# Kernel optimization log

Measured on AMD Instinct MI355X. Metric: run time of the kernel, lower is better.

Reference implementation:

```python
import jax, jax.numpy as jnp
import numpy as np

B, N = 4, 512
C_IN, H, W = 1024, 48, 48
IMG_H, IMG_W = 48.0, 48.0
CNN_EMB, BOX_EMB, GCN_OUT = 512, 256, 512
ROWS, COLS = 58, 30
ALPHA = 5.0
K_EDGES = 8 * N  # edges kept per image per graph

# all directed pairs (i != j) of a fully-connected graph on N nodes
_ii, _jj = np.meshgrid(np.arange(N), np.arange(N), indexing='ij')
_m = _ii != _jj
PAIRS = jnp.asarray(np.stack([_ii[_m], _jj[_m]], axis=1).astype(np.int32))  # [E,2]


def setup_inputs():
    key = jax.random.key(0)
    ks = jax.random.split(key, 12)
    x = jax.random.normal(ks[0], (B, C_IN, H, W), jnp.float32)
    # valid boxes (x1<x2, y1<y2) inside the 48x48 feature map
    p = jax.random.uniform(ks[1], (B, N, 2, 2), minval=0.0, maxval=float(W) - 2.0)
    lo = jnp.min(p, axis=2)
    hi = jnp.max(p, axis=2) + 1.0
    boxes = jnp.concatenate([lo, hi], axis=-1)  # [B,N,4] x1,y1,x2,y2

    def lin(k, fi, fo):
        return jax.random.normal(k, (fi, fo), jnp.float32) / np.sqrt(fi)

    return {
        'input': x, 'boxes': boxes,
        'im_scales': jnp.ones((B,), jnp.float32),
        'pdls': jnp.zeros((B,), jnp.float32),
        'pdts': jnp.zeros((B,), jnp.float32),
        'W_dec': jax.random.normal(ks[2], (256, C_IN, 3, 3), jnp.float32) / np.sqrt(C_IN * 9.0),
        'b_dec': jnp.zeros((256,), jnp.float32),
        'W_box': lin(ks[3], 4, BOX_EMB), 'b_box': jnp.zeros((BOX_EMB,), jnp.float32),
        'W_cnn': lin(ks[4], 256 * 4, CNN_EMB), 'b_cnn': jnp.zeros((CNN_EMB,), jnp.float32),
        'W_grow': lin(ks[5], CNN_EMB + BOX_EMB, GCN_OUT), 'b_grow': jnp.zeros((GCN_OUT,), jnp.float32),
        'W_gcol': lin(ks[6], CNN_EMB + BOX_EMB, GCN_OUT), 'b_gcol': jnp.zeros((GCN_OUT,), jnp.float32),
        'W_rcls': lin(ks[7], GCN_OUT, 2 * (ROWS - 1) * 2), 'b_rcls': jnp.zeros((2 * (ROWS - 1) * 2,), jnp.float32),
        'W_ccls': lin(ks[8], GCN_OUT, 2 * (COLS - 1) * 2), 'b_ccls': jnp.zeros((2 * (COLS - 1) * 2,), jnp.float32),
    }


def _bilinear(feat, bidx, py, px):
    # feat [B,C,H,W]; py,px [M,4] sample coords -> [M,4,C]
    Hh, Ww = feat.shape[2], feat.shape[3]
    py = jnp.clip(py, 0.0, Hh - 1.0)
    px = jnp.clip(px, 0.0, Ww - 1.0)
    y0 = jnp.floor(py).astype(jnp.int32)
    x0 = jnp.floor(px).astype(jnp.int32)
    y1 = jnp.minimum(y0 + 1, Hh - 1)
    x1 = jnp.minimum(x0 + 1, Ww - 1)
    wy = (py - y0)[..., None]
    wx = (px - x0)[..., None]
    b = bidx[:, None]
    f00 = feat[b, :, y0, x0]
    f01 = feat[b, :, y0, x1]
    f10 = feat[b, :, y1, x0]
    f11 = feat[b, :, y1, x1]
    return f00 * (1 - wy) * (1 - wx) + f01 * (1 - wy) * wx + f10 * wy * (1 - wx) + f11 * wy * wx


def _roi_align_2x2(feat, boxes, bidx):
    # roi_align output_size=2, spatial_scale=1, one sample per bin (bin center)
    x1, y1, x2, y2 = boxes[:, 0], boxes[:, 1], boxes[:, 2], boxes[:, 3]
    bw = (x2 - x1) / 2.0
    bh = (y2 - y1) / 2.0
    offs = jnp.array([0.5, 1.5], jnp.float32)
    sx = x1[:, None] + offs * bw[:, None]  # [M,2]
    sy = y1[:, None] + offs * bh[:, None]
    py = sy[:, jnp.array([0, 0, 1, 1])]  # (iy, ix) ordering
    px = sx[:, jnp.array([0, 1, 0, 1])]
    val = _bilinear(feat, bidx, py, px)  # [M,4,C]
    return jnp.transpose(val, (0, 2, 1)).reshape(val.shape[0], -1)  # [M, C*2*2]


def _edge_attrs(boxes_i, scale, pdl, pdt):
    org = (boxes_i - jnp.stack([pdl, pdt, pdl, pdt])) / scale
    cx = (org[:, 0] + org[:, 2]) * 0.5
    cy = (org[:, 1] + org[:, 3]) * 0.5
    tb_w = jnp.max(org[:, jnp.array([0, 2])])
    tb_h = jnp.max(org[:, jnp.array([1, 3])])
    s, d = PAIRS[:, 0], PAIRS[:, 1]
    row_attr = jnp.exp(-jnp.square((cy[s] - cy[d]) * ALPHA / tb_h))
    col_attr = jnp.exp(-jnp.square((cx[s] - cx[d]) * ALPHA / tb_w))
    rv, ri = jax.lax.top_k(row_attr, K_EDGES)
    cv, ci = jax.lax.top_k(col_attr, K_EDGES)
    return rv, PAIRS[ri], cv, PAIRS[ci]


def _gcn(x, Wg, bg, edges, ew, num_nodes):
    # PyG GCNConv: self-loops with weight 1, symmetric normalization
    loop = jnp.arange(num_nodes, dtype=edges.dtype)
    src = jnp.concatenate([edges[0], loop])
    dst = jnp.concatenate([edges[1], loop])
    w = jnp.concatenate([ew, jnp.ones((num_nodes,), ew.dtype)])
    deg = jax.ops.segment_sum(w, dst, num_segments=num_nodes)
    dis = jax.lax.rsqrt(deg)  # deg >= 1 thanks to self-loops
    norm = dis[src] * w * dis[dst]
    xw = x @ Wg
    agg = jax.ops.segment_sum(norm[:, None] * xw[src], dst, num_segments=num_nodes)
    return agg + bg


def _forward(input, boxes, im_scales, pdls, pdts, W_dec, b_dec, W_box, b_box,
             W_cnn, b_cnn, W_grow, b_grow, W_gcol, b_gcol, W_rcls, b_rcls, W_ccls, b_ccls):
    Bn = B * N
    flat = boxes.reshape(Bn, 4)
    # box features (relative center / size)
    cx = (flat[:, 0] + flat[:, 2]) / 2.0
    cy = (flat[:, 1] + flat[:, 3]) / 2.0
    bf = jnp.stack([cx / IMG_W, cy / IMG_H,
                    (flat[:, 2] - flat[:, 0]) / IMG_W,
                    (flat[:, 3] - flat[:, 1]) / IMG_H], axis=1)
    box_feat = jax.nn.relu(bf @ W_box + b_box)
    # decode conv + relu
    dec = jax.lax.conv_general_dilated(input, W_dec, (1, 1), 'SAME',
                                       dimension_numbers=('NCHW', 'OIHW', 'NCHW'))
    dec = jax.nn.relu(dec + b_dec[None, :, None, None])
    # roi-align 2x2 + cnn embedding
    bidx = jnp.repeat(jnp.arange(B, dtype=jnp.int32), N)
    cnn = _roi_align_2x2(dec, flat, bidx)
    cnn_feat = jax.nn.relu(cnn @ W_cnn + b_cnn)
    # per-image dense graph -> top-8N row/col edges
    rv, re, cv, ce = jax.vmap(_edge_attrs)(boxes, im_scales, pdls, pdts)
    off = (jnp.arange(B, dtype=jnp.int32) * N)[:, None, None]
    row_edge = (re + off).reshape(-1, 2).T  # [2, B*K]
    col_edge = (ce + off).reshape(-1, 2).T
    row_w = rv.reshape(-1)
    col_w = cv.reshape(-1)
    fusion = jnp.concatenate([box_feat, cnn_feat], axis=1)  # [Bn, 768]
    row_feat = jax.nn.relu(_gcn(fusion, W_grow, b_grow, row_edge, row_w, Bn))
    col_feat = jax.nn.relu(_gcn(fusion, W_gcol, b_gcol, col_edge, col_w, Bn))
    row_score = jax.nn.leaky_relu(row_feat @ W_rcls + b_rcls, 0.01).reshape(Bn, 2, ROWS - 1, 2)
    col_score = jax.nn.leaky_relu(col_feat @ W_ccls + b_ccls, 0.01).reshape(Bn, 2, COLS - 1, 2)
    return row_score, col_score


def reference(input, boxes, im_scales, pdls, pdts, W_dec, b_dec, W_box, b_box,
              W_cnn, b_cnn, W_grow, b_grow, W_gcol, b_gcol, W_rcls, b_rcls, W_ccls, b_ccls):
    return _forward(input, boxes, im_scales, pdls, pdts, W_dec, b_dec, W_box, b_box,
                    W_cnn, b_cnn, W_grow, b_grow, W_gcol, b_gcol,
                    W_rcls, b_rcls, W_ccls, b_ccls)
```

## Files before the change

kernel.cpp:

```cpp
#include <hip/hip_runtime.h>
#include <cstdint>
#include <math.h>

typedef unsigned int u32;
typedef unsigned long long u64;
typedef unsigned short ushort;

typedef __attribute__((ext_vector_type(8))) _Float16 f16x8;
typedef __attribute__((ext_vector_type(4))) _Float16 f16x4;
typedef __attribute__((ext_vector_type(4))) float f32x4;

#define NB    4
#define BnN   2048
#define NE    261632
#define NCHUNK 32
#define ECHUNK 8176
#define KEDGE 4096
#define TIECAP 2048
#define PSLICE 2359296
#define MS    64
#define TS    64

#define GLD16(gsrc, ldst)                                                    \
    __builtin_amdgcn_global_load_lds(                                        \
        (const __attribute__((address_space(1))) void*)(gsrc),               \
        (__attribute__((address_space(3))) void*)(ldst), 16, 0, 0)

__global__ __launch_bounds__(256) void prep_kernel(
    const float* __restrict__ in, _Float16* __restrict__ xf,
    const float* __restrict__ W, _Float16* __restrict__ wf,
    const float* __restrict__ Wc,  _Float16* __restrict__ WcT,
    const float* __restrict__ Wgr, _Float16* __restrict__ WgrT,
    const float* __restrict__ Wgc, _Float16* __restrict__ WgcT,
    const float* __restrict__ Wr,  _Float16* __restrict__ WrT,
    const float* __restrict__ Wcc, _Float16* __restrict__ WccT)
{
    __shared__ _Float16 sh[9216];
    const int bid = blockIdx.x;
    const int tid = threadIdx.x;
    if (bid < 3072) {
        _Float16 (*shx)[49] = (_Float16(*)[49])sh;
        int cg = bid & 15, rem = bid >> 4;
        int y = rem % 48, b = rem / 48;
        for (int i = tid; i < 64 * 48; i += 256) {
            int cl = i / 48, x = i - cl * 48;
            shx[cl][x] = (_Float16)in[(((size_t)b * 1024 + cg * 64 + cl) * 48 + y) * 48 + x];
        }
        __syncthreads();
        for (int i = tid; i < 64 * 48; i += 256) {
            int x = i / 64, cl = i - x * 64;
            xf[((size_t)(b * 48 + y) * 48 + x) * 1024 + cg * 64 + cl] = shx[cl][x];
        }
    } else if (bid < 3328) {
        int o = bid - 3072;
        for (int g = tid; g < 9216; g += 256)
            sh[g] = (_Float16)W[(size_t)o * 9216 + g];
        __syncthreads();
        for (int g = tid; g < 9216; g += 256) {
            int tap = g >> 10, ch = g & 1023;
            wf[(size_t)o * 9216 + g] = sh[ch * 9 + tap];
        }
    } else {
        _Float16 (*sht)[33] = (_Float16(*)[33])sh;
        int b2 = bid - 3328;
        const float* inm; _Float16* outm; int K, N, tx0, ty0, ntx;
        if (b2 < 512)       { inm = Wc;  outm = WcT;  K = 1024; N = 512; ntx = 16; b2 -= 0;    }
        else if (b2 < 896)  { inm = Wgr; outm = WgrT; K = 768;  N = 512; ntx = 16; b2 -= 512;  }
        else if (b2 < 1280) { inm = Wgc; outm = WgcT; K = 768;  N = 512; ntx = 16; b2 -= 896;  }
        else if (b2 < 1408) { inm = Wr;  outm = WrT;  K = 512;  N = 228; ntx = 8;  b2 -= 1280; }
        else                { inm = Wcc; outm = WccT; K = 512;  N = 116; ntx = 4;  b2 -= 1408; }
        tx0 = (b2 % ntx) * 32;
        ty0 = (b2 / ntx) * 32;
        int tx = tid & 31, ty = tid >> 5;
#pragma unroll
        for (int i = 0; i < 4; ++i) {
            int k = ty0 + ty + i * 8, n = tx0 + tx;
            sht[ty + i * 8][tx] = (k < K && n < N) ? (_Float16)inm[(size_t)k * N + n] : (_Float16)0.f;
        }
        __syncthreads();
#pragma unroll
        for (int i = 0; i < 4; ++i) {
            int n = tx0 + ty + i * 8, k = ty0 + tx;
            if (n < N && k < K) outm[(size_t)n * K + k] = sht[tx][ty + i * 8];
        }
    }
}

#define STAGE(cc)                                                            \
    {                                                                        \
        _Pragma("unroll")                                                    \
        for (int it = 0; it < 5; ++it) {                                     \
            if (it * 256 + wv * 64 < 1152)                                   \
                GLD16(wsrc[it] + (cc), &wS[(it * 256 + wv * 64) * 8]);       \
        }                                                                    \
        _Pragma("unroll")                                                    \
        for (int it = 0; it < 8; ++it)                                       \
            GLD16(xsrc[it] + (cc), &xS[(it * 256 + wv * 64) * 8]);           \
    }

#define LDB(BUF, R)                                                          \
    {                                                                        \
        _Pragma("unroll")                                                    \
        for (int u = 0; u < 9; ++u) {                                        \
            int nt_ = u / 3, dx_ = u % 3;                                    \
            BUF[u] = *(const f16x8*)&xS[(((R) * 4 + q) * 50 + nt_ * 16 + n + dx_) * 8]; \
        }                                                                    \
    }

#define DOTAP(TAP, BLO, BHI)                                                 \
    {                                                                        \
        _Pragma("unroll")                                                    \
        for (int dx_ = 0; dx_ < 3; ++dx_) {                                  \
            f16x8 a0 = *(const f16x8*)&wS[(((TAP) + dx_) * 128 + q * 32 + n) * 8];      \
            f16x8 a1 = *(const f16x8*)&wS[(((TAP) + dx_) * 128 + q * 32 + 16 + n) * 8]; \
            _Pragma("unroll")                                                \
            for (int nt_ = 0; nt_ < 3; ++nt_) {                              \
                f16x8 blo = BLO[nt_ * 3 + dx_];                              \
                f16x8 bhi = BHI[nt_ * 3 + dx_];                              \
                acc[0][0][nt_] = __builtin_amdgcn_mfma_f32_16x16x32_f16(a0, blo, acc[0][0][nt_], 0, 0, 0); \
                acc[1][0][nt_] = __builtin_amdgcn_mfma_f32_16x16x32_f16(a1, blo, acc[1][0][nt_], 0, 0, 0); \
                acc[0][1][nt_] = __builtin_amdgcn_mfma_f32_16x16x32_f16(a0, bhi, acc[0][1][nt_], 0, 0, 0); \
                acc[1][1][nt_] = __builtin_amdgcn_mfma_f32_16x16x32_f16(a1, bhi, acc[1][1][nt_], 0, 0, 0); \
            }                                                                \
        }                                                                    \
    }

__global__ __launch_bounds__(256, 3) void conv_part_kernel(
    const _Float16* __restrict__ xf, const _Float16* __restrict__ wf,
    const _Float16* __restrict__ zbuf, float* __restrict__ pbuf)
{
    __shared__ _Float16 wS[1152 * 8];
    __shared__ _Float16 xS[2048 * 8];
    const int p = blockIdx.x;
    const int L = (p & 7) * 96 + (p >> 3);
    const int og = L & 7;
    const int t  = L >> 3;
    const int xt = t % 6;
    const int bz = t / 6;
    const int y0 = xt * 8;
    const int b  = bz >> 2, ks = bz & 3;
    const int tid = threadIdx.x;
    const int wv = tid >> 6;
    const int ln = tid & 63;
    const int n  = ln & 15;
    const int q  = ln >> 4;

    f32x4 acc[2][2][3];
#pragma unroll
    for (int mt = 0; mt < 2; ++mt)
#pragma unroll
        for (int rr = 0; rr < 2; ++rr)
#pragma unroll
            for (int nt = 0; nt < 3; ++nt) acc[mt][rr][nt] = (f32x4){0.f, 0.f, 0.f, 0.f};

    const _Float16* wsrc[5];
    const _Float16* xsrc[8];
#pragma unroll
    for (int it = 0; it < 5; ++it) {
        int g = it * 256 + tid;
        int gg = (g < 1152) ? g : 0;
        int tap = gg >> 7, r = gg & 127, qq = r >> 5, oc = r & 31;
        wsrc[it] = wf + (size_t)(((og * 32 + oc) * 9 + tap) * 1024 + qq * 8);
    }
#pragma unroll
    for (int it = 0; it < 8; ++it) {
        int g = it * 256 + tid;
        int row = g / 200, r2 = g - row * 200;
        int qq = r2 / 50, c = r2 - qq * 50;
        int gy = y0 + row - 1, gx = c - 1;
        bool inb = (g < 2000) && ((unsigned)gy < 48u) && ((unsigned)gx < 48u);
        xsrc[it] = inb ? (xf + (size_t)(((b * 48 + gy) * 48 + gx) * 1024 + qq * 8)) : zbuf;
    }

    const int c0 = ks * 256;
    const int rbase = 2 * wv;

    STAGE(c0);

#pragma unroll 1
    for (int ci = 0; ci < 8; ++ci) {
        asm volatile("s_waitcnt vmcnt(0)" ::: "memory");
        __syncthreads();

        __builtin_amdgcn_s_setprio(1);
        f16x8 bA[9], bB[9];
        LDB(bA, rbase + 0);
        LDB(bB, rbase + 1);
        DOTAP(0, bA, bB);
        LDB(bA, rbase + 2);
        DOTAP(3, bB, bA);
        LDB(bB, rbase + 3);
        DOTAP(6, bA, bB);
        __builtin_amdgcn_s_setprio(0);
        __syncthreads();
        if (ci < 7) STAGE(c0 + (ci + 1) * 32);
    }

#pragma unroll
    for (int rr = 0; rr < 2; ++rr) {
        const int y = y0 + 2 * wv + rr;
#pragma unroll
        for (int mt = 0; mt < 2; ++mt) {
#pragma unroll
            for (int nt = 0; nt < 3; ++nt) {
                int x = nt * 16 + n;
                *(f32x4*)(pbuf + (size_t)ks * PSLICE +
                          ((size_t)(b * 48 + y) * 48 + x) * 256 + og * 32 + mt * 16 + q * 4) = acc[mt][rr][nt];
            }
        }
    }
}

__global__ __launch_bounds__(256) void conv_sum_kernel(
    const float* __restrict__ pbuf, const float* __restrict__ bd,
    _Float16* __restrict__ dec)
{
    size_t idx = (size_t)blockIdx.x * 256 + threadIdx.x;
    size_t e = idx * 4;
    int och = (int)(e & 255);
    f32x4 s0 = *(const f32x4*)(pbuf + e);
    f32x4 s1 = *(const f32x4*)(pbuf + (size_t)PSLICE + e);
    f32x4 s2 = *(const f32x4*)(pbuf + (size_t)2 * PSLICE + e);
    f32x4 s3 = *(const f32x4*)(pbuf + (size_t)3 * PSLICE + e);
    float4 b4 = *(const float4*)(bd + och);
    f16x4 v;
    v.x = (_Float16)fmaxf(s0[0] + s1[0] + s2[0] + s3[0] + b4.x, 0.f);
    v.y = (_Float16)fmaxf(s0[1] + s1[1] + s2[1] + s3[1] + b4.y, 0.f);
    v.z = (_Float16)fmaxf(s0[2] + s1[2] + s2[2] + s3[2] + b4.z, 0.f);
    v.w = (_Float16)fmaxf(s0[3] + s1[3] + s2[3] + s3[3] + b4.w, 0.f);
    *(f16x4*)(dec + e) = v;
}

__global__ __launch_bounds__(256) void roi_box_kernel(
    const _Float16* __restrict__ dec, const float* __restrict__ boxes,
    const float* __restrict__ Wb, const float* __restrict__ bb,
    _Float16* __restrict__ cnn, _Float16* __restrict__ fusion)
{
    int n = blockIdx.x; int c = threadIdx.x;
    int b = n >> 9;
    float x1 = boxes[n * 4 + 0], y1 = boxes[n * 4 + 1];
    float x2 = boxes[n * 4 + 2], y2 = boxes[n * 4 + 3];
    {
        float bf0 = ((x1 + x2) * 0.5f) / 48.f;
        float bf1 = ((y1 + y2) * 0.5f) / 48.f;
        float bf2 = (x2 - x1) / 48.f;
        float bf3 = (y2 - y1) / 48.f;
        float acc = bb[c];
        acc += bf0 * Wb[0 * 256 + c];
        acc += bf1 * Wb[1 * 256 + c];
        acc += bf2 * Wb[2 * 256 + c];
        acc += bf3 * Wb[3 * 256 + c];
        fusion[(size_t)n * 768 + c] = (_Float16)fmaxf(acc, 0.f);
    }
    float bw = (x2 - x1) * 0.5f, bh = (y2 - y1) * 0.5f;
    float sxv[2] = { x1 + 0.5f * bw, x1 + 1.5f * bw };
    float syv[2] = { y1 + 0.5f * bh, y1 + 1.5f * bh };
    float px[4] = { sxv[0], sxv[1], sxv[0], sxv[1] };
    float py[4] = { syv[0], syv[0], syv[1], syv[1] };
    const _Float16* f = dec + (size_t)b * 2304 * 256;
    f16x4 o4;
    float res[4];
#pragma unroll
    for (int p = 0; p < 4; ++p) {
        float yy = fminf(fmaxf(py[p], 0.f), 47.f);
        float xx = fminf(fmaxf(px[p], 0.f), 47.f);
        int y0 = (int)floorf(yy), x0 = (int)floorf(xx);
        int y1i = min(y0 + 1, 47), x1i = min(x0 + 1, 47);
        float wy = yy - (float)y0, wx = xx - (float)x0;
        float f00 = (float)f[(size_t)(y0 * 48 + x0) * 256 + c];
        float f01 = (float)f[(size_t)(y0 * 48 + x1i) * 256 + c];
        float f10 = (float)f[(size_t)(y1i * 48 + x0) * 256 + c];
        float f11 = (float)f[(size_t)(y1i * 48 + x1i) * 256 + c];
        res[p] = f00 * (1.f - wy) * (1.f - wx) + f01 * (1.f - wy) * wx
               + f10 * wy * (1.f - wx) + f11 * wy * wx;
    }
    o4.x = (_Float16)res[0]; o4.y = (_Float16)res[1];
    o4.z = (_Float16)res[2]; o4.w = (_Float16)res[3];
    *(f16x4*)(cnn + (size_t)n * 1024 + c * 4) = o4;
}

#define GEMM_STAGE(cc, bi)                                                   \
    {                                                                        \
        GLD16(asrc + (cc), &aS[bi][(wv * 64) * 8]);                          \
        GLD16(bsrc + (cc), &bS[bi][(wv * 64) * 8]);                          \
    }

template <int ACT, typename OUTT>
__global__ __launch_bounds__(256) void gemm16_kernel(
    const _Float16* __restrict__ A, const _Float16* __restrict__ Bt,
    const _Float16* __restrict__ zbuf,
    const float* __restrict__ bias, OUTT* __restrict__ C,
    int M, int N, int K, int ldC)
{
    __shared__ _Float16 aS[2][256 * 8];
    __shared__ _Float16 bS[2][256 * 8];
    const int n0 = blockIdx.x * 64, m0 = blockIdx.y * 64;
    const int tid = threadIdx.x;
    const int wv = tid >> 6, ln = tid & 63;
    const int wm = wv & 1, wn = wv >> 1;
    const int lm = ln & 15, lq = ln >> 4;
    const int sr = tid >> 2, sq = tid & 3;

    const _Float16* asrc = A + (size_t)(m0 + sr) * K + sq * 8;
    const _Float16* bsrc = (n0 + sr < N) ? (Bt + (size_t)(n0 + sr) * K + sq * 8) : zbuf;

    f32x4 acc[2][2];
#pragma unroll
    for (int i = 0; i < 2; ++i)
#pragma unroll
        for (int j = 0; j < 2; ++j) acc[i][j] = (f32x4){0.f, 0.f, 0.f, 0.f};

    const int NT = K >> 5;
    GEMM_STAGE(0, 0);
#pragma unroll 1
    for (int it = 0; it < NT; ++it) {
        const int bi = it & 1;
        if (it + 1 < NT) {
            GEMM_STAGE((it + 1) * 32, bi ^ 1);
            asm volatile("s_waitcnt vmcnt(2)" ::: "memory");
        } else {
            asm volatile("s_waitcnt vmcnt(0)" ::: "memory");
        }
        __builtin_amdgcn_s_barrier();
        f16x8 af[2], bf[2];
#pragma unroll
        for (int mt = 0; mt < 2; ++mt) af[mt] = *(const f16x8*)&aS[bi][(wm * 32 + mt * 16 + lm) * 32 + lq * 8];
#pragma unroll
        for (int nt = 0; nt < 2; ++nt) bf[nt] = *(const f16x8*)&bS[bi][(wn * 32 + nt * 16 + lm) * 32 + lq * 8];
#pragma unroll
        for (int mt = 0; mt < 2; ++mt)
#pragma unroll
            for (int nt = 0; nt < 2; ++nt)
                acc[mt][nt] = __builtin_amdgcn_mfma_f32_16x16x32_f16(af[mt], bf[nt], acc[mt][nt], 0, 0, 0);
        __builtin_amdgcn_sched_barrier(0);
        __builtin_amdgcn_s_barrier();
    }

#pragma unroll
    for (int mt = 0; mt < 2; ++mt) {
#pragma unroll
        for (int nt = 0; nt < 2; ++nt) {
            int col = n0 + wn * 32 + nt * 16 + lm;
            if (col >= N) continue;
            float bs = bias ? bias[col] : 0.f;
#pragma unroll
            for (int r = 0; r < 4; ++r) {
                int row = m0 + wm * 32 + mt * 16 + lq * 4 + r;
                float v = acc[mt][nt][r] + bs;
                if (ACT == 1) v = fmaxf(v, 0.f);
                if (ACT == 2) v = (v >= 0.f) ? v : 0.01f * v;
                C[(size_t)row * ldC + col] = (OUTT)v;
            }
        }
    }
}

__global__ __launch_bounds__(256) void gemm16z_kernel(
    const _Float16* __restrict__ A,
    const _Float16* __restrict__ Bt0, const _Float16* __restrict__ Bt1,
    const _Float16* __restrict__ zbuf,
    float* __restrict__ C0, float* __restrict__ C1,
    int M, int N, int K, int ldC)
{
    const _Float16* __restrict__ Bt = blockIdx.z ? Bt1 : Bt0;
    float* __restrict__ C = blockIdx.z ? C1 : C0;
    __shared__ _Float16 aS[2][256 * 8];
    __shared__ _Float16 bS[2][256 * 8];
    const int n0 = blockIdx.x * 64, m0 = blockIdx.y * 64;
    const int tid = threadIdx.x;
    const int wv = tid >> 6, ln = tid & 63;
    const int wm = wv & 1, wn = wv >> 1;
    const int lm = ln & 15, lq = ln >> 4;
    const int sr = tid >> 2, sq = tid & 3;

    const _Float16* asrc = A + (size_t)(m0 + sr) * K + sq * 8;
    const _Float16* bsrc = (n0 + sr < N) ? (Bt + (size_t)(n0 + sr) * K + sq * 8) : zbuf;

    f32x4 acc[2][2];
#pragma unroll
    for (int i = 0; i < 2; ++i)
#pragma unroll
        for (int j = 0; j < 2; ++j) acc[i][j] = (f32x4){0.f, 0.f, 0.f, 0.f};

    const int NT = K >> 5;
    GEMM_STAGE(0, 0);
#pragma unroll 1
    for (int it = 0; it < NT; ++it) {
        const int bi = it & 1;
        if (it + 1 < NT) {
            GEMM_STAGE((it + 1) * 32, bi ^ 1);
            asm volatile("s_waitcnt vmcnt(2)" ::: "memory");
        } else {
            asm volatile("s_waitcnt vmcnt(0)" ::: "memory");
        }
        __builtin_amdgcn_s_barrier();
        f16x8 af[2], bf[2];
#pragma unroll
        for (int mt = 0; mt < 2; ++mt) af[mt] = *(const f16x8*)&aS[bi][(wm * 32 + mt * 16 + lm) * 32 + lq * 8];
#pragma unroll
        for (int nt = 0; nt < 2; ++nt) bf[nt] = *(const f16x8*)&bS[bi][(wn * 32 + nt * 16 + lm) * 32 + lq * 8];
#pragma unroll
        for (int mt = 0; mt < 2; ++mt)
#pragma unroll
            for (int nt = 0; nt < 2; ++nt)
                acc[mt][nt] = __builtin_amdgcn_mfma_f32_16x16x32_f16(af[mt], bf[nt], acc[mt][nt], 0, 0, 0);
        __builtin_amdgcn_sched_barrier(0);
        __builtin_amdgcn_s_barrier();
    }

#pragma unroll
    for (int mt = 0; mt < 2; ++mt) {
#pragma unroll
        for (int nt = 0; nt < 2; ++nt) {
            int col = n0 + wn * 32 + nt * 16 + lm;
            if (col >= N) continue;
#pragma unroll
            for (int r = 0; r < 4; ++r) {
                int row = m0 + wm * 32 + mt * 16 + lq * 4 + r;
                C[(size_t)row * ldC + col] = acc[mt][nt][r];
            }
        }
    }
}

__global__ __launch_bounds__(256) void gemm16h_kernel(
    const _Float16* __restrict__ A0, const _Float16* __restrict__ A1,
    const _Float16* __restrict__ Bt0, const _Float16* __restrict__ Bt1,
    const _Float16* __restrict__ zbuf,
    const float* __restrict__ bias0, const float* __restrict__ bias1,
    float* __restrict__ C0, float* __restrict__ C1,
    int M, int N0, int N1, int K)
{
    const int z = blockIdx.z;
    const _Float16* __restrict__ A  = z ? A1 : A0;
    const _Float16* __restrict__ Bt = z ? Bt1 : Bt0;
    const float* __restrict__ bias  = z ? bias1 : bias0;
    float* __restrict__ C           = z ? C1 : C0;
    const int N = z ? N1 : N0;
    const int ldC = N;
    const int n0 = blockIdx.x * 64, m0 = blockIdx.y * 64;
    if (n0 >= N) return;
    __shared__ _Float16 aS[2][256 * 8];
    __shared__ _Float16 bS[2][256 * 8];
    const int tid = threadIdx.x;
    const int wv = tid >> 6, ln = tid & 63;
    const int wm = wv & 1, wn = wv >> 1;
    const int lm = ln & 15, lq = ln >> 4;
    const int sr = tid >> 2, sq = tid & 3;

    const _Float16* asrc = A + (size_t)(m0 + sr) * K + sq * 8;
    const _Float16* bsrc = (n0 + sr < N) ? (Bt + (size_t)(n0 + sr) * K + sq * 8) : zbuf;

    f32x4 acc[2][2];
#pragma unroll
    for (int i = 0; i < 2; ++i)
#pragma unroll
        for (int j = 0; j < 2; ++j) acc[i][j] = (f32x4){0.f, 0.f, 0.f, 0.f};

    const int NT = K >> 5;
    GEMM_STAGE(0, 0);
#pragma unroll 1
    for (int it = 0; it < NT; ++it) {
        const int bi = it & 1;
        if (it + 1 < NT) {
            GEMM_STAGE((it + 1) * 32, bi ^ 1);
            asm volatile("s_waitcnt vmcnt(2)" ::: "memory");
        } else {
            asm volatile("s_waitcnt vmcnt(0)" ::: "memory");
        }
        __builtin_amdgcn_s_barrier();
        f16x8 af[2], bf[2];
#pragma unroll
        for (int mt = 0; mt < 2; ++mt) af[mt] = *(const f16x8*)&aS[bi][(wm * 32 + mt * 16 + lm) * 32 + lq * 8];
#pragma unroll
        for (int nt = 0; nt < 2; ++nt) bf[nt] = *(const f16x8*)&bS[bi][(wn * 32 + nt * 16 + lm) * 32 + lq * 8];
#pragma unroll
        for (int mt = 0; mt < 2; ++mt)
#pragma unroll
            for (int nt = 0; nt < 2; ++nt)
                acc[mt][nt] = __builtin_amdgcn_mfma_f32_16x16x32_f16(af[mt], bf[nt], acc[mt][nt], 0, 0, 0);
        __builtin_amdgcn_sched_barrier(0);
        __builtin_amdgcn_s_barrier();
    }

#pragma unroll
    for (int mt = 0; mt < 2; ++mt) {
#pragma unroll
        for (int nt = 0; nt < 2; ++nt) {
            int col = n0 + wn * 32 + nt * 16 + lm;
            if (col >= N) continue;
            float bs = bias[col];
#pragma unroll
            for (int r = 0; r < 4; ++r) {
                int row = m0 + wm * 32 + mt * 16 + lq * 4 + r;
                float v = acc[mt][nt][r] + bs;
                v = (v >= 0.f) ? v : 0.01f * v;
                C[(size_t)row * ldC + col] = v;
            }
        }
    }
}

__device__ __forceinline__ float compute_sv_tb(
    const float* __restrict__ boxes, const float* __restrict__ scales,
    const float* __restrict__ pdls, const float* __restrict__ pdts,
    int b, int t, float* sv, float* red)
{
    int tid = threadIdx.x;
    float pdl = pdls[b], pdt = pdts[b], sc = scales[b];
    if (tid < 512) {
        const float* bx = boxes + (size_t)(b * 512 + tid) * 4;
        float o0 = (bx[0] - pdl) / sc;
        float o1 = (bx[1] - pdt) / sc;
        float o2 = (bx[2] - pdl) / sc;
        float o3 = (bx[3] - pdt) / sc;
        sv[tid]  = (t == 0) ? (o1 + o3) * 0.5f : (o0 + o2) * 0.5f;
        red[tid] = (t == 0) ? fmaxf(o1, o3)    : fmaxf(o0, o2);
    }
    __syncthreads();
    for (int s = 256; s > 0; s >>= 1) {
        if (tid < s) red[tid] = fmaxf(red[tid], red[tid + s]);
        __syncthreads();
    }
    float tbv = red[0];
    __syncthreads();
    return tbv;
}

#define QBITS(e, QB)                                                   \
    {                                                                  \
        int i_ = (e) / 511; int jj_ = (e) - i_ * 511;                  \
        int j_ = jj_ + (jj_ >= i_ ? 1 : 0);                            \
        float diff_ = sv[i_] - sv[j_];                                 \
        float u_ = (diff_ * 5.0f) / tbv;                               \
        float q_ = u_ * u_;                                            \
        QB = __float_as_uint(q_);                                      \
    }

__global__ __launch_bounds__(1024) void histA_kernel(
    const float* __restrict__ boxes, const float* __restrict__ scales,
    const float* __restrict__ pdls, const float* __restrict__ pdts,
    u32* __restrict__ gpart)
{
    __shared__ float sv[512]; __shared__ float red[512];
    __shared__ u32 lh[4096];
    const int sel = blockIdx.y, b = sel >> 1, t = sel & 1;
    const int tid = threadIdx.x;
    for (int i = tid; i < 4096; i += 1024) lh[i] = 0;
    const float tbv = compute_sv_tb(boxes, scales, pdls, pdts, b, t, sv, red);
    const int e1 = min((int)(blockIdx.x + 1) * ECHUNK, NE);
    for (int e = blockIdx.x * ECHUNK + tid; e < e1; e += 1024) {
        u32 qb; QBITS(e, qb);
        atomicAdd(&lh[qb >> 20], 1u);
    }
    __syncthreads();
    u32* G = gpart + ((size_t)sel * NCHUNK + blockIdx.x) * 4096;
    for (int i = tid; i < 4096; i += 1024) G[i] = lh[i];
}

__global__ __launch_bounds__(1024) void scanA_kernel(
    const u32* __restrict__ gpart, u32* __restrict__ meta)
{
    const int sel = blockIdx.x, tid = threadIdx.x;
    __shared__ u32 bins[4096];
    __shared__ u32 sc[2][1024];
    for (int b = tid; b < 4096; b += 1024) {
        u32 s = 0;
        for (int c = 0; c < NCHUNK; ++c) s += gpart[((size_t)sel * NCHUNK + c) * 4096 + b];
        bins[b] = s;
    }
    __syncthreads();
    u32 part = 0;
#pragma unroll
    for (int j = 0; j < 4; ++j) part += bins[tid * 4 + j];
    sc[0][tid] = part;
    __syncthreads();
    int src = 0;
    for (int st = 1; st < 1024; st <<= 1) {
        sc[1 - src][tid] = sc[src][tid] + (tid >= st ? sc[src][tid - st] : 0);
        __syncthreads(); src = 1 - src;
    }
    u32 inc = sc[src][tid], exc = inc - part;
    if (exc < (u32)KEDGE && (u32)KEDGE <= inc) {
        u32 cum = exc;
        for (int j = 0; j < 4; ++j) {
            u32 c = bins[tid * 4 + j];
            if (cum + c >= (u32)KEDGE) {
                meta[sel * MS + 0] = (u32)(tid * 4 + j);
                meta[sel * MS + 1] = (u32)KEDGE - cum;
                break;
            }
            cum += c;
        }
    }
}

__global__ __launch_bounds__(1024) void histB_kernel(
    const float* __restrict__ boxes, const float* __restrict__ scales,
    const float* __restrict__ pdls, const float* __restrict__ pdts,
    const u32* __restrict__ meta, u32* __restrict__ gpart)
{
    __shared__ float sv[512]; __shared__ float red[512];
    __shared__ u32 lh[4096];
    const int sel = blockIdx.y, b = sel >> 1, t = sel & 1;
    const int tid = threadIdx.x;
    for (int i = tid; i < 4096; i += 1024) lh[i] = 0;
    const float tbv = compute_sv_tb(boxes, scales, pdls, pdts, b, t, sv, red);
    const u32 p12 = meta[sel * MS + 0];
    const int e1 = min((int)(blockIdx.x + 1) * ECHUNK, NE);
    for (int e = blockIdx.x * ECHUNK + tid; e < e1; e += 1024) {
        u32 qb; QBITS(e, qb);
        if ((qb >> 20) == p12) atomicAdd(&lh[(qb >> 8) & 0xFFF], 1u);
    }
    __syncthreads();
    u32* G = gpart + ((size_t)sel * NCHUNK + blockIdx.x) * 4096;
    for (int i = tid; i < 4096; i += 1024) G[i] = lh[i];
}

__global__ __launch_bounds__(1024) void scanB_kernel(
    const u32* __restrict__ gpart, u32* __restrict__ meta)
{
    const int sel = blockIdx.x, tid = threadIdx.x;
    const u32 TH = meta[sel * MS + 1];
    __shared__ u32 bins[4096];
    __shared__ u32 sc[2][1024];
    for (int b = tid; b < 4096; b += 1024) {
        u32 s = 0;
        for (int c = 0; c < NCHUNK; ++c) s += gpart[((size_t)sel * NCHUNK + c) * 4096 + b];
        bins[b] = s;
    }
    __syncthreads();
    u32 part = 0;
#pragma unroll
    for (int j = 0; j < 4; ++j) part += bins[tid * 4 + j];
    sc[0][tid] = part;
    __syncthreads();
    int src = 0;
    for (int st = 1; st < 1024; st <<= 1) {
        sc[1 - src][tid] = sc[src][tid] + (tid >= st ? sc[src][tid - st] : 0);
        __syncthreads(); src = 1 - src;
    }
    u32 inc = sc[src][tid], exc = inc - part;
    if (exc < TH && TH <= inc) {
        u32 cum = exc;
        for (int j = 0; j < 4; ++j) {
            u32 c = bins[tid * 4 + j];
            if (cum + c >= TH) {
                meta[sel * MS + 6] = (meta[sel * MS + 0] << 12) | (u32)(tid * 4 + j);
                meta[sel * MS + 7] = TH - cum;
                break;
            }
            cum += c;
        }
    }
}

__global__ __launch_bounds__(1024) void histC_kernel(
    const float* __restrict__ boxes, const float* __restrict__ scales,
    const float* __restrict__ pdls, const float* __restrict__ pdts,
    const u32* __restrict__ meta, u32* __restrict__ gpart)
{
    __shared__ float sv[512]; __shared__ float red[512];
    __shared__ u32 lh[256];
    const int sel = blockIdx.y, b = sel >> 1, t = sel & 1;
    const int tid = threadIdx.x;
    if (tid < 256) lh[tid] = 0;
    const float tbv = compute_sv_tb(boxes, scales, pdls, pdts, b, t, sv, red);
    const u32 p24 = meta[sel * MS + 6];
    const int e1 = min((int)(blockIdx.x + 1) * ECHUNK, NE);
    for (int e = blockIdx.x * ECHUNK + tid; e < e1; e += 1024) {
        u32 qb; QBITS(e, qb);
        if ((qb >> 8) == p24) atomicAdd(&lh[qb & 0xFF], 1u);
    }
    __syncthreads();
    u32* G = gpart + ((size_t)sel * NCHUNK + blockIdx.x) * 256;
    if (tid < 256) G[tid] = lh[tid];
}

__global__ __launch_bounds__(256) void scanC_kernel(
    const u32* __restrict__ gpart, u32* __restrict__ meta)
{
    const int sel = blockIdx.x, tid = threadIdx.x;
    const u32 TH = meta[sel * MS + 7];
    __shared__ u32 bins[256];
    __shared__ u32 sc[2][256];
    __shared__ u32 s_qstar;
    u32 s = 0;
    for (int c = 0; c < NCHUNK; ++c) s += gpart[((size_t)sel * NCHUNK + c) * 256 + tid];
    bins[tid] = s;
    sc[0][tid] = s;
    __syncthreads();
    int src = 0;
    for (int st = 1; st < 256; st <<= 1) {
        sc[1 - src][tid] = sc[src][tid] + (tid >= st ? sc[src][tid - st] : 0);
        __syncthreads(); src = 1 - src;
    }
    u32 inc = sc[src][tid], exc = inc - bins[tid];
    if (exc < TH && TH <= inc)
        s_qstar = (meta[sel * MS + 6] << 8) | (u32)tid;
    __syncthreads();
    if (tid == 0) {
        u32 prefix = s_qstar;
        float qstar = __uint_as_float(prefix);
        float wstar = (float)exp(-(double)qstar);
        u32 lo = 0, hi = prefix;
        while (lo < hi) {
            u32 mid = (lo + hi) >> 1;
            float wm = (float)exp(-(double)__uint_as_float(mid));
            if (wm > wstar) lo = mid + 1; else hi = mid;
        }
        meta[sel * MS + 2] = lo;
        lo = prefix; hi = 0x7F800000u;
        while (lo < hi) {
            u32 mid = (lo + hi + 1) >> 1;
            float wm = (float)exp(-(double)__uint_as_float(mid));
            if (wm < wstar) hi = mid - 1; else lo = mid;
        }
        meta[sel * MS + 3] = lo;
        meta[sel * MS + 4] = __float_as_uint(wstar);
    }
}

__global__ __launch_bounds__(1024) void emit_kernel(
    const float* __restrict__ boxes, const float* __restrict__ scales,
    const float* __restrict__ pdls, const float* __restrict__ pdts,
    u32* __restrict__ meta, int* __restrict__ tiebuf, int* __restrict__ tiecnt,
    int* __restrict__ es, int* __restrict__ ed, float* __restrict__ ewt,
    int* __restrict__ indeg, float* __restrict__ degw)
{
    __shared__ float sv[512]; __shared__ float red[512];
    __shared__ int s_wcnt, s_tcnt, s_wbase, s_tbase;
    const int sel = blockIdx.y, b = sel >> 1, t = sel & 1;
    const int tid = threadIdx.x;
    const float tbv = compute_sv_tb(boxes, scales, pdls, pdts, b, t, sv, red);
    const u32 qlo = meta[sel * MS + 2], qhi = meta[sel * MS + 3];
    const int base = t * 16384 + b * 4096;
    const int e0 = blockIdx.x * ECHUNK + tid;
    const int e1 = min((int)(blockIdx.x + 1) * ECHUNK, NE);
    if (tid == 0) { s_wcnt = 0; s_tcnt = 0; }
    __syncthreads();
    int myw = 0, myt = 0;
    for (int e = e0; e < e1; e += 1024) {
        u32 qb; QBITS(e, qb);
        if (qb < qlo) ++myw;
        else if (qb <= qhi) ++myt;
    }
    if (myw) atomicAdd(&s_wcnt, myw);
    if (myt) atomicAdd(&s_tcnt, myt);
    __syncthreads();
    if (tid == 0) {
        s_wbase = (s_wcnt > 0) ? (int)atomicAdd(&meta[sel * MS + 5], (u32)s_wcnt) : 0;
        s_tbase = (s_tcnt > 0) ? atomicAdd(&tiecnt[sel * TS], s_tcnt) : 0;
        s_wcnt = 0; s_tcnt = 0;
    }
    __syncthreads();
    for (int e = e0; e < e1; e += 1024) {
        u32 qb; QBITS(e, qb);
        if (qb < qlo) {
            int i = e / 511; int jj = e - i * 511; int j = jj + (jj >= i ? 1 : 0);
            float wval = (float)exp(-(double)__uint_as_float(qb));
            int slot = s_wbase + atomicAdd(&s_wcnt, 1);
            es[base + slot] = b * 512 + i;
            ed[base + slot] = b * 512 + j;
            ewt[base + slot] = wval;
            atomicAdd(&indeg[t * 2048 + b * 512 + j], 1);
            atomicAdd(&degw[t * 2048 + b * 512 + j], wval);
        } else if (qb <= qhi) {
            int p = s_tbase + atomicAdd(&s_tcnt, 1);
            if (p < TIECAP) tiebuf[sel * TIECAP + p] = e;
        }
    }
}

__global__ __launch_bounds__(1024) void tie_scan_fill_kernel(
    u32* __restrict__ meta, const int* __restrict__ tiebuf, const int* __restrict__ tiecnt,
    int* __restrict__ es, int* __restrict__ ed, float* __restrict__ ewt,
    int* __restrict__ indeg, float* __restrict__ degw,
    int* __restrict__ offs, float* __restrict__ dis, int* __restrict__ csr)
{
    __shared__ int bufA[2048], bufB[2048];
    __shared__ int fill_l[2048];
    const int t = blockIdx.x, tid = threadIdx.x;
    for (int b = 0; b < 4; ++b) {
        int sel = b * 2 + t;
        int m = min(tiecnt[sel * TS], TIECAP);
        int r = KEDGE - (int)meta[sel * MS + 5];
        float wt = __uint_as_float(meta[sel * MS + 4]);
        int base = t * 16384 + b * 4096;
        for (int k = tid; k < m; k += 1024) {
            int e = tiebuf[sel * TIECAP + k];
            int rank = 0;
            for (int l = 0; l < m; ++l) rank += (tiebuf[sel * TIECAP + l] < e) ? 1 : 0;
            if (rank < r) {
                int i = e / 511; int jj = e - i * 511; int j = jj + (jj >= i ? 1 : 0);
                int slot = (int)atomicAdd(&meta[sel * MS + 5], 1u);
                es[base + slot] = b * 512 + i;
                ed[base + slot] = b * 512 + j;
                ewt[base + slot] = wt;
                atomicAdd(&indeg[t * 2048 + b * 512 + j], 1);
                atomicAdd(&degw[t * 2048 + b * 512 + j], wt);
            }
        }
    }
    __threadfence();
    __syncthreads();
    bufA[tid] = indeg[t * 2048 + tid];
    bufA[tid + 1024] = indeg[t * 2048 + tid + 1024];
    fill_l[tid] = 0; fill_l[tid + 1024] = 0;
    __syncthreads();
    int* src = bufA; int* dst = bufB;
    for (int st = 1; st < 2048; st <<= 1) {
        dst[tid] = src[tid] + (tid >= st ? src[tid - st] : 0);
        int k1 = tid + 1024;
        dst[k1] = src[k1] + (k1 >= st ? src[k1 - st] : 0);
        __syncthreads();
        int* tmp = src; src = dst; dst = tmp;
    }
    int off0 = (tid == 0) ? 0 : src[tid - 1];
    int off1 = src[tid + 1023];
    __syncthreads();
    dst[tid] = off0; dst[tid + 1024] = off1;
    offs[t * 2048 + tid] = off0;
    offs[t * 2048 + tid + 1024] = off1;
    dis[t * 2048 + tid] = 1.0f / sqrtf(1.0f + degw[t * 2048 + tid]);
    dis[t * 2048 + tid + 1024] = 1.0f / sqrtf(1.0f + degw[t * 2048 + tid + 1024]);
    __syncthreads();
    for (int e = tid; e < 16384; e += 1024) {
        int dl = ed[t * 16384 + e] & 2047;
        int pos = dst[dl] + atomicAdd(&fill_l[dl], 1);
        csr[t * 16384 + pos] = e;
    }
}

__global__ __launch_bounds__(256) void gcn_agg_kernel(
    const float* __restrict__ xw_row, const float* __restrict__ xw_col,
    const float* __restrict__ b_row, const float* __restrict__ b_col,
    const int* __restrict__ es, const float* __restrict__ ew,
    const int* __restrict__ csr, const int* __restrict__ offs,
    const int* __restrict__ indeg, const float* __restrict__ dis,
    _Float16* __restrict__ feat_row, _Float16* __restrict__ feat_col)
{
    int d = blockIdx.x; int t = blockIdx.y;
    const float* xw = t ? xw_col : xw_row;
    const float* bg = t ? b_col : b_row;
    _Float16* out = t ? feat_col : feat_row;
    int f0 = threadIdx.x, f1 = threadIdx.x + 256;
    float dd = dis[t * 2048 + d];
    float a0 = dd * dd * xw[(size_t)d * 512 + f0];
    float a1 = dd * dd * xw[(size_t)d * 512 + f1];
    int st = offs[t * 2048 + d], cnt = indeg[t * 2048 + d];
    for (int k = 0; k < cnt; ++k) {
        int e = csr[t * 16384 + st + k];
        int s = es[t * 16384 + e];
        float w = ew[t * 16384 + e];
        float coef = dis[t * 2048 + s] * w * dd;
        a0 += coef * xw[(size_t)s * 512 + f0];
        a1 += coef * xw[(size_t)s * 512 + f1];
    }
    a0 += bg[f0]; a1 += bg[f1];
    out[(size_t)d * 512 + f0] = (_Float16)fmaxf(a0, 0.f);
    out[(size_t)d * 512 + f1] = (_Float16)fmaxf(a1, 0.f);
}

extern "C" void kernel_launch(void* const* d_in, const int* in_sizes, int n_in,
                              void* d_out, int out_size, void* d_ws, size_t ws_size,
                              hipStream_t stream)
{
    const float* x      = (const float*)d_in[0];
    const float* boxes  = (const float*)d_in[1];
    const float* scales = (const float*)d_in[2];
    const float* pdls   = (const float*)d_in[3];
    const float* pdts   = (const float*)d_in[4];
    const float* W_dec  = (const float*)d_in[5];
    const float* b_dec  = (const float*)d_in[6];
    const float* W_box  = (const float*)d_in[7];
    const float* b_box  = (const float*)d_in[8];
    const float* W_cnn  = (const float*)d_in[9];
    const float* b_cnn  = (const float*)d_in[10];
    const float* W_grow = (const float*)d_in[11];
    const float* b_grow = (const float*)d_in[12];
    const float* W_gcol = (const float*)d_in[13];
    const float* b_gcol = (const float*)d_in[14];
    const float* W_rcls = (const float*)d_in[15];
    const float* b_rcls = (const float*)d_in[16];
    const float* W_ccls = (const float*)d_in[17];
    const float* b_ccls = (const float*)d_in[18];

    char* ws = (char*)d_ws;
    size_t off = 0;
    auto alloc = [&](size_t bytes) -> void* {
        void* p = ws + off;
        off = (off + bytes + 255) & ~(size_t)255;
        return p;
    };
    _Float16* xf16   = (_Float16*)alloc((size_t)4 * 2304 * 1024 * 2);
    _Float16* wf16   = (_Float16*)alloc((size_t)256 * 9216 * 2);
    _Float16* dec    = (_Float16*)alloc((size_t)4 * 2304 * 256 * 2);
    float*    pbuf   = (float*)   alloc((size_t)4 * PSLICE * 4);
    _Float16* cnn    = (_Float16*)alloc((size_t)2048 * 1024 * 2);
    _Float16* fusion = (_Float16*)alloc((size_t)2048 * 768 * 2);
    _Float16* WcT    = (_Float16*)alloc((size_t)512 * 1024 * 2);
    _Float16* WgrT   = (_Float16*)alloc((size_t)512 * 768 * 2);
    _Float16* WgcT   = (_Float16*)alloc((size_t)512 * 768 * 2);
    _Float16* WrT    = (_Float16*)alloc((size_t)228 * 512 * 2);
    _Float16* WccT   = (_Float16*)alloc((size_t)116 * 512 * 2);
    float* xw        = (float*)alloc((size_t)2097152 * 4);
    _Float16* feats  = (_Float16*)alloc((size_t)2 * 2048 * 512 * 2);
    int*  es     = (int*)  alloc((size_t)2 * 16384 * 4);
    int*  ed     = (int*)  alloc((size_t)2 * 16384 * 4);
    float* ewt   = (float*)alloc((size_t)2 * 16384 * 4);
    int*  offsA  = (int*)  alloc((size_t)4096 * 4);
    float* dis   = (float*)alloc((size_t)4096 * 4);
    int*  csr    = (int*)  alloc((size_t)2 * 16384 * 4);
    int*  tiebuf = (int*)  alloc((size_t)8 * TIECAP * 4);
    u32*  gpartA = (u32*)  alloc((size_t)8 * NCHUNK * 4096 * 4);
    u32*  gpartB = (u32*)  alloc((size_t)8 * NCHUNK * 4096 * 4);
    u32*  gpartC = (u32*)  alloc((size_t)8 * NCHUNK * 256 * 4);
    size_t z0 = off;
    u32*  meta   = (u32*)  alloc((size_t)8 * MS * 4);
    int*  tiecnt = (int*)  alloc((size_t)8 * TS * 4);
    int*  indeg  = (int*)  alloc((size_t)4096 * 4);
    float* degw  = (float*)alloc((size_t)4096 * 4);
    _Float16* zbuf = (_Float16*)alloc((size_t)4096);
    size_t z1 = off;

    float* out = (float*)d_out;

    hipMemsetAsync(ws + z0, 0, z1 - z0, stream);

    prep_kernel<<<4800, 256, 0, stream>>>(x, xf16, W_dec, wf16,
                                          W_cnn, WcT, W_grow, WgrT, W_gcol, WgcT,
                                          W_rcls, WrT, W_ccls, WccT);
    conv_part_kernel<<<dim3(768), 256, 0, stream>>>(xf16, wf16, zbuf, pbuf);
    conv_sum_kernel<<<2304, 256, 0, stream>>>(pbuf, b_dec, dec);
    roi_box_kernel<<<2048, 256, 0, stream>>>(dec, boxes, W_box, b_box, cnn, fusion);
    gemm16_kernel<1, _Float16><<<dim3(8, 32), 256, 0, stream>>>(cnn, WcT, zbuf, b_cnn, fusion + 256, 2048, 512, 1024, 768);
    histA_kernel<<<dim3(NCHUNK, 8), 1024, 0, stream>>>(boxes, scales, pdls, pdts, gpartA);
    scanA_kernel<<<8, 1024, 0, stream>>>(gpartA, meta);
    histB_kernel<<<dim3(NCHUNK, 8), 1024, 0, stream>>>(boxes, scales, pdls, pdts, meta, gpartB);
    scanB_kernel<<<8, 1024, 0, stream>>>(gpartB, meta);
    histC_kernel<<<dim3(NCHUNK, 8), 1024, 0, stream>>>(boxes, scales, pdls, pdts, meta, gpartC);
    scanC_kernel<<<8, 256, 0, stream>>>(gpartC, meta);
    emit_kernel<<<dim3(NCHUNK, 8), 1024, 0, stream>>>(boxes, scales, pdls, pdts, meta,
                                                      tiebuf, tiecnt, es, ed, ewt, indeg, degw);
    tie_scan_fill_kernel<<<2, 1024, 0, stream>>>(meta, tiebuf, tiecnt, es, ed, ewt,
                                                 indeg, degw, offsA, dis, csr);
    gemm16z_kernel<<<dim3(8, 32, 2), 256, 0, stream>>>(fusion, WgrT, WgcT, zbuf, xw, xw + 1048576,
                                                       2048, 512, 768, 512);
    gcn_agg_kernel<<<dim3(2048, 2), 256, 0, stream>>>(xw, xw + 1048576, b_grow, b_gcol,
                                                      es, ewt, csr, offsA, indeg, dis,
                                                      feats, feats + (size_t)2048 * 512);
    gemm16h_kernel<<<dim3(4, 32, 2), 256, 0, stream>>>(feats, feats + (size_t)2048 * 512,
                                                       WrT, WccT, zbuf, b_rcls, b_ccls,
                                                       out, out + (size_t)2048 * 228,
                                                       2048, 228, 116, 512);
}
```

Baseline: 346.5 us.

## Co-schedule edge top-k histogram passes with CNN/GEMM kernels in merged launches

The independent top-k edge-selection chain (histA/scanA/histB/scanB/histC) is interleaved with the dense feature pipeline. Extra blocks are appended to the conv, conv-sum, ROI, CNN-GEMM and GCN-GEMM launches so each launch also runs one histogram or scan stage. The goal is to remove five serial launches and fill idle CUs while the dense kernels run. The histogram and scan bodies are rewritten for 256-thread blocks, and the conv kernel now uses a larger shared-memory union, which could lower its occupancy.

After: 410.8 us. 1.19x slower.

```diff
diff --git a/kernel.cpp b/kernel.cpp
--- a/kernel.cpp
+++ b/kernel.cpp
@@ -82,6 +82,205 @@
         for (int i = 0; i < 4; ++i) {
             int n = tx0 + ty + i * 8, k = ty0 + tx;
             if (n < N && k < K) outm[(size_t)n * K + k] = sht[tx][ty + i * 8];
+        }
+    }
+}
+
+__device__ __forceinline__ float sv_tb_256(
+    const float* __restrict__ boxes, const float* __restrict__ scales,
+    const float* __restrict__ pdls, const float* __restrict__ pdts,
+    int b, int t, float* sv, float* red)
+{
+    int tid = threadIdx.x;
+    float pdl = pdls[b], pdt = pdts[b], sc = scales[b];
+    for (int r = tid; r < 512; r += 256) {
+        const float* bx = boxes + (size_t)(b * 512 + r) * 4;
+        float o0 = (bx[0] - pdl) / sc;
+        float o1 = (bx[1] - pdt) / sc;
+        float o2 = (bx[2] - pdl) / sc;
+        float o3 = (bx[3] - pdt) / sc;
+        sv[r]  = (t == 0) ? (o1 + o3) * 0.5f : (o0 + o2) * 0.5f;
+        red[r] = (t == 0) ? fmaxf(o1, o3)    : fmaxf(o0, o2);
+    }
+    __syncthreads();
+    red[tid] = fmaxf(red[tid], red[tid + 256]);
+    __syncthreads();
+    for (int s = 128; s > 0; s >>= 1) {
+        if (tid < s) red[tid] = fmaxf(red[tid], red[tid + s]);
+        __syncthreads();
+    }
+    float tbv = red[0];
+    __syncthreads();
+    return tbv;
+}
+
+#define QBITS(e, QB)                                                   \
+    {                                                                  \
+        int i_ = (e) / 511; int jj_ = (e) - i_ * 511;                  \
+        int j_ = jj_ + (jj_ >= i_ ? 1 : 0);                            \
+        float diff_ = sv[i_] - sv[j_];                                 \
+        float u_ = (diff_ * 5.0f) / tbv;                               \
+        float q_ = u_ * u_;                                            \
+        QB = __float_as_uint(q_);                                      \
+    }
+
+__device__ __forceinline__ void hist12_256(
+    const float* __restrict__ boxes, const float* __restrict__ scales,
+    const float* __restrict__ pdls, const float* __restrict__ pdts,
+    u32* __restrict__ gpart, int h, char* smem,
+    int pass , const u32* __restrict__ meta)
+{
+    float* sv = (float*)smem; float* red = (float*)(smem + 2048);
+    u32* lh = (u32*)(smem + 4096);
+    const int sel = h >> 5, chunk = h & 31, b = sel >> 1, t = sel & 1;
+    const int tid = threadIdx.x;
+    for (int i = tid; i < 4096; i += 256) lh[i] = 0;
+    const float tbv = sv_tb_256(boxes, scales, pdls, pdts, b, t, sv, red);
+    const u32 p12 = pass ? meta[sel * MS + 0] : 0u;
+    const int e1 = min((chunk + 1) * ECHUNK, NE);
+    for (int e = chunk * ECHUNK + tid; e < e1; e += 256) {
+        u32 qb; QBITS(e, qb);
+        if (pass == 0) atomicAdd(&lh[qb >> 20], 1u);
+        else if ((qb >> 20) == p12) atomicAdd(&lh[(qb >> 8) & 0xFFF], 1u);
+    }
+    __syncthreads();
+    u32* G = gpart + ((size_t)sel * NCHUNK + chunk) * 4096;
+    for (int i = tid; i < 4096; i += 256) G[i] = lh[i];
+}
+
+__device__ __forceinline__ void scan12_256(
+    const u32* __restrict__ gpart, u32* __restrict__ meta, int sel,
+    char* smem, int pass)
+{
+    u32* bins = (u32*)smem;
+    u32* sc2  = (u32*)(smem + 16384);
+    const int tid = threadIdx.x;
+    const u32 TH = pass ? meta[sel * MS + 1] : (u32)KEDGE;
+    for (int bb = tid; bb < 4096; bb += 256) {
+        u32 s = 0;
+        for (int c = 0; c < NCHUNK; ++c) s += gpart[((size_t)sel * NCHUNK + c) * 4096 + bb];
+        bins[bb] = s;
+    }
+    __syncthreads();
+    u32 part = 0;
+#pragma unroll
+    for (int j = 0; j < 16; ++j) part += bins[tid * 16 + j];
+    sc2[tid] = part;
+    __syncthreads();
+    int src = 0;
+    for (int st = 1; st < 256; st <<= 1) {
+        sc2[(1 - src) * 256 + tid] = sc2[src * 256 + tid] + (tid >= st ? sc2[src * 256 + tid - st] : 0);
+        __syncthreads(); src = 1 - src;
+    }
+    u32 inc = sc2[src * 256 + tid], exc = inc - part;
+    if (exc < TH && TH <= inc) {
+        u32 cum = exc;
+        for (int j = 0; j < 16; ++j) {
+            u32 c = bins[tid * 16 + j];
+            if (cum + c >= TH) {
+                if (pass == 0) {
+                    meta[sel * MS + 0] = (u32)(tid * 16 + j);
+                    meta[sel * MS + 1] = TH - cum;
+                } else {
+                    meta[sel * MS + 6] = (meta[sel * MS + 0] << 12) | (u32)(tid * 16 + j);
+                    meta[sel * MS + 7] = TH - cum;
+                }
+                break;
+            }
+            cum += c;
+        }
+    }
+}
+
+__device__ __forceinline__ void histC_256(
+    const float* __restrict__ boxes, const float* __restrict__ scales,
+    const float* __restrict__ pdls, const float* __restrict__ pdts,
+    const u32* __restrict__ meta, u32* __restrict__ gpart, int h, char* smem)
+{
+    float* sv = (float*)smem; float* red = (float*)(smem + 2048);
+    u32* lh = (u32*)(smem + 4096);
+    const int sel = h >> 5, chunk = h & 31, b = sel >> 1, t = sel & 1;
+    const int tid = threadIdx.x;
+    lh[tid] = 0;
+    const float tbv = sv_tb_256(boxes, scales, pdls, pdts, b, t, sv, red);
+    const u32 p24 = meta[sel * MS + 6];
+    const int e1 = min((chunk + 1) * ECHUNK, NE);
+    for (int e = chunk * ECHUNK + tid; e < e1; e += 256) {
+        u32 qb; QBITS(e, qb);
+        if ((qb >> 8) == p24) atomicAdd(&lh[qb & 0xFF], 1u);
+    }
+    __syncthreads();
+    u32* G = gpart + ((size_t)sel * NCHUNK + chunk) * 256;
+    G[tid] = lh[tid];
+}
+
+template <int ACT, typename OUTT>
+__device__ __forceinline__ void gemm_body(
+    const _Float16* __restrict__ A, const _Float16* __restrict__ Bt,
+    const _Float16* __restrict__ zbuf, const float* __restrict__ bias,
+    OUTT* __restrict__ C, int N, int K, int ldC, int n0, int m0,
+    _Float16* aSp, _Float16* bSp)
+{
+    const int tid = threadIdx.x;
+    const int wv = tid >> 6, ln = tid & 63;
+    const int wm = wv & 1, wn = wv >> 1;
+    const int lm = ln & 15, lq = ln >> 4;
+    const int sr = tid >> 2, sq = tid & 3;
+
+    const _Float16* asrc = A + (size_t)(m0 + sr) * K + sq * 8;
+    const _Float16* bsrc = (n0 + sr < N) ? (Bt + (size_t)(n0 + sr) * K + sq * 8) : zbuf;
+
+    f32x4 acc[2][2];
+#pragma unroll
+    for (int i = 0; i < 2; ++i)
+#pragma unroll
+        for (int j = 0; j < 2; ++j) acc[i][j] = (f32x4){0.f, 0.f, 0.f, 0.f};
+
+    const int NT = K >> 5;
+    GLD16(asrc, aSp + wv * 512);
+    GLD16(bsrc, bSp + wv * 512);
+#pragma unroll 1
+    for (int it = 0; it < NT; ++it) {
+        const int bi = it & 1;
+        if (it + 1 < NT) {
+            GLD16(asrc + (it + 1) * 32, aSp + (bi ^ 1) * 2048 + wv * 512);
+            GLD16(bsrc + (it + 1) * 32, bSp + (bi ^ 1) * 2048 + wv * 512);
+            asm volatile("s_waitcnt vmcnt(2)" ::: "memory");
+        } else {
+            asm volatile("s_waitcnt vmcnt(0)" ::: "memory");
+        }
+        __builtin_amdgcn_s_barrier();
+        f16x8 af[2], bf[2];
+#pragma unroll
+        for (int mt = 0; mt < 2; ++mt)
+            af[mt] = *(const f16x8*)(aSp + bi * 2048 + (wm * 32 + mt * 16 + lm) * 32 + lq * 8);
+#pragma unroll
+        for (int nt = 0; nt < 2; ++nt)
+            bf[nt] = *(const f16x8*)(bSp + bi * 2048 + (wn * 32 + nt * 16 + lm) * 32 + lq * 8);
+#pragma unroll
+        for (int mt = 0; mt < 2; ++mt)
+#pragma unroll
+            for (int nt = 0; nt < 2; ++nt)
+                acc[mt][nt] = __builtin_amdgcn_mfma_f32_16x16x32_f16(af[mt], bf[nt], acc[mt][nt], 0, 0, 0);
+        __builtin_amdgcn_sched_barrier(0);
+        __builtin_amdgcn_s_barrier();
+    }
+
+#pragma unroll
+    for (int mt = 0; mt < 2; ++mt) {
+#pragma unroll
+        for (int nt = 0; nt < 2; ++nt) {
+            int col = n0 + wn * 32 + nt * 16 + lm;
+            if (col >= N) continue;
+            float bs = bias ? bias[col] : 0.f;
+#pragma unroll
+            for (int r = 0; r < 4; ++r) {
+                int row = m0 + wm * 32 + mt * 16 + lq * 4 + r;
+                float v = acc[mt][nt][r] + bs;
+                if (ACT == 1) v = fmaxf(v, 0.f);
+                if (ACT == 2) v = (v >= 0.f) ? v : 0.01f * v;
+                C[(size_t)row * ldC + col] = (OUTT)v;
+            }
         }
     }
 }
@@ -125,13 +324,23 @@
         }                                                                    \
     }
 
-__global__ __launch_bounds__(256, 3) void conv_part_kernel(
+__global__ __launch_bounds__(256, 3) void conv_histA_kernel(
     const _Float16* __restrict__ xf, const _Float16* __restrict__ wf,
-    const _Float16* __restrict__ zbuf, float* __restrict__ pbuf)
-{
-    __shared__ _Float16 wS[1152 * 8];
-    __shared__ _Float16 xS[2048 * 8];
-    const int p = blockIdx.x;
+    const _Float16* __restrict__ zbuf, float* __restrict__ pbuf,
+    const float* __restrict__ boxes, const float* __restrict__ scales,
+    const float* __restrict__ pdls, const float* __restrict__ pdts,
+    u32* __restrict__ gpartA)
+{
+    __shared__ __attribute__((aligned(16))) char smem[51200];
+    const int bid = blockIdx.x;
+    const int tid = threadIdx.x;
+    if (bid >= 768) {
+        hist12_256(boxes, scales, pdls, pdts, gpartA, bid - 768, smem, 0, nullptr);
+        return;
+    }
+    _Float16* wS = (_Float16*)smem;
+    _Float16* xS = (_Float16*)(smem + 18432);
+    const int p = bid;
     const int L = (p & 7) * 96 + (p >> 3);
     const int og = L & 7;
     const int t  = L >> 3;
@@ -139,7 +348,6 @@
     const int bz = t / 6;
     const int y0 = xt * 8;
     const int b  = bz >> 2, ks = bz & 3;
-    const int tid = threadIdx.x;
     const int wv = tid >> 6;
     const int ln = tid & 63;
     const int n  = ln & 15;
@@ -211,11 +419,15 @@
     }
 }
 
-__global__ __launch_bounds__(256) void conv_sum_kernel(
+__global__ __launch_bounds__(256) void sum_scanA_kernel(
     const float* __restrict__ pbuf, const float* __restrict__ bd,
-    _Float16* __restrict__ dec)
-{
-    size_t idx = (size_t)blockIdx.x * 256 + threadIdx.x;
+    _Float16* __restrict__ dec, const u32* __restrict__ gpartA,
+    u32* __restrict__ meta)
+{
+    __shared__ __attribute__((aligned(16))) char smem[18432];
+    const int bid = blockIdx.x;
+    if (bid >= 2304) { scan12_256(gpartA, meta, bid - 2304, smem, 0); return; }
+    size_t idx = (size_t)bid * 256 + threadIdx.x;
     size_t e = idx * 4;
     int och = (int)(e & 255);
     f32x4 s0 = *(const f32x4*)(pbuf + e);
@@ -231,12 +443,21 @@
     *(f16x4*)(dec + e) = v;
 }
 
-__global__ __launch_bounds__(256) void roi_box_kernel(
+__global__ __launch_bounds__(256) void roi_histB_kernel(
     const _Float16* __restrict__ dec, const float* __restrict__ boxes,
     const float* __restrict__ Wb, const float* __restrict__ bb,
-    _Float16* __restrict__ cnn, _Float16* __restrict__ fusion)
-{
-    int n = blockIdx.x; int c = threadIdx.x;
+    _Float16* __restrict__ cnn, _Float16* __restrict__ fusion,
+    const float* __restrict__ scales, const float* __restrict__ pdls,
+    const float* __restrict__ pdts, const u32* __restrict__ meta,
+    u32* __restrict__ gpartB)
+{
+    __shared__ __attribute__((aligned(16))) char smem[20480];
+    const int nblk = blockIdx.x;
+    if (nblk >= 2048) {
+        hist12_256(boxes, scales, pdls, pdts, gpartB, nblk - 2048, smem, 1, meta);
+        return;
+    }
+    int n = nblk; int c = threadIdx.x;
     int b = n >> 9;
     float x1 = boxes[n * 4 + 0], y1 = boxes[n * 4 + 1];
     float x2 = boxes[n * 4 + 2], y2 = boxes[n * 4 + 3];
@@ -279,148 +500,40 @@
     *(f16x4*)(cnn + (size_t)n * 1024 + c * 4) = o4;
 }
 
-#define GEMM_STAGE(cc, bi)                                                   \
-    {                                                                        \
-        GLD16(asrc + (cc), &aS[bi][(wv * 64) * 8]);                          \
-        GLD16(bsrc + (cc), &bS[bi][(wv * 64) * 8]);                          \
-    }
-
-template <int ACT, typename OUTT>
-__global__ __launch_bounds__(256) void gemm16_kernel(
-    const _Float16* __restrict__ A, const _Float16* __restrict__ Bt,
-    const _Float16* __restrict__ zbuf,
-    const float* __restrict__ bias, OUTT* __restrict__ C,
-    int M, int N, int K, int ldC)
-{
-    __shared__ _Float16 aS[2][256 * 8];
-    __shared__ _Float16 bS[2][256 * 8];
-    const int n0 = blockIdx.x * 64, m0 = blockIdx.y * 64;
-    const int tid = threadIdx.x;
-    const int wv = tid >> 6, ln = tid & 63;
-    const int wm = wv & 1, wn = wv >> 1;
-    const int lm = ln & 15, lq = ln >> 4;
-    const int sr = tid >> 2, sq = tid & 3;
-
-    const _Float16* asrc = A + (size_t)(m0 + sr) * K + sq * 8;
-    const _Float16* bsrc = (n0 + sr < N) ? (Bt + (size_t)(n0 + sr) * K + sq * 8) : zbuf;
-
-    f32x4 acc[2][2];
-#pragma unroll
-    for (int i = 0; i < 2; ++i)
-#pragma unroll
-        for (int j = 0; j < 2; ++j) acc[i][j] = (f32x4){0.f, 0.f, 0.f, 0.f};
-
-    const int NT = K >> 5;
-    GEMM_STAGE(0, 0);
-#pragma unroll 1
-    for (int it = 0; it < NT; ++it) {
-        const int bi = it & 1;
-        if (it + 1 < NT) {
-            GEMM_STAGE((it + 1) * 32, bi ^ 1);
-            asm volatile("s_waitcnt vmcnt(2)" ::: "memory");
-        } else {
-            asm volatile("s_waitcnt vmcnt(0)" ::: "memory");
-        }
-        __builtin_amdgcn_s_barrier();
-        f16x8 af[2], bf[2];
-#pragma unroll
-        for (int mt = 0; mt < 2; ++mt) af[mt] = *(const f16x8*)&aS[bi][(wm * 32 + mt * 16 + lm) * 32 + lq * 8];
-#pragma unroll
-        for (int nt = 0; nt < 2; ++nt) bf[nt] = *(const f16x8*)&bS[bi][(wn * 32 + nt * 16 + lm) * 32 + lq * 8];
-#pragma unroll
-        for (int mt = 0; mt < 2; ++mt)
-#pragma unroll
-            for (int nt = 0; nt < 2; ++nt)
-                acc[mt][nt] = __builtin_amdgcn_mfma_f32_16x16x32_f16(af[mt], bf[nt], acc[mt][nt], 0, 0, 0);
-        __builtin_amdgcn_sched_barrier(0);
-        __builtin_amdgcn_s_barrier();
-    }
-
-#pragma unroll
-    for (int mt = 0; mt < 2; ++mt) {
-#pragma unroll
-        for (int nt = 0; nt < 2; ++nt) {
-            int col = n0 + wn * 32 + nt * 16 + lm;
-            if (col >= N) continue;
-            float bs = bias ? bias[col] : 0.f;
-#pragma unroll
-            for (int r = 0; r < 4; ++r) {
-                int row = m0 + wm * 32 + mt * 16 + lq * 4 + r;
-                float v = acc[mt][nt][r] + bs;
-                if (ACT == 1) v = fmaxf(v, 0.f);
-                if (ACT == 2) v = (v >= 0.f) ? v : 0.01f * v;
-                C[(size_t)row * ldC + col] = (OUTT)v;
-            }
-        }
-    }
-}
-
-__global__ __launch_bounds__(256) void gemm16z_kernel(
-    const _Float16* __restrict__ A,
-    const _Float16* __restrict__ Bt0, const _Float16* __restrict__ Bt1,
+__global__ __launch_bounds__(256) void gemmcnn_scanB_kernel(
+    const _Float16* __restrict__ cnn, const _Float16* __restrict__ WcT,
+    const _Float16* __restrict__ zbuf, const float* __restrict__ b_cnn,
+    _Float16* __restrict__ fusionC, const u32* __restrict__ gpartB,
+    u32* __restrict__ meta)
+{
+    __shared__ __attribute__((aligned(16))) char smem[18432];
+    const int bid = blockIdx.x;
+    if (bid >= 256) { scan12_256(gpartB, meta, bid - 256, smem, 1); return; }
+    const int n0 = (bid & 7) * 64, m0 = (bid >> 3) * 64;
+    gemm_body<1, _Float16>(cnn, WcT, zbuf, b_cnn, fusionC, 512, 1024, 768, n0, m0,
+                           (_Float16*)smem, (_Float16*)(smem + 8192));
+}
+
+__global__ __launch_bounds__(256) void gemmz_histC_kernel(
+    const _Float16* __restrict__ fusion,
+    const _Float16* __restrict__ WgrT, const _Float16* __restrict__ WgcT,
     const _Float16* __restrict__ zbuf,
     float* __restrict__ C0, float* __restrict__ C1,
-    int M, int N, int K, int ldC)
-{
-    const _Float16* __restrict__ Bt = blockIdx.z ? Bt1 : Bt0;
-    float* __restrict__ C = blockIdx.z ? C1 : C0;
-    __shared__ _Float16 aS[2][256 * 8];
-    __shared__ _Float16 bS[2][256 * 8];
-    const int n0 = blockIdx.x * 64, m0 = blockIdx.y * 64;
-    const int tid = threadIdx.x;
-    const int wv = tid >> 6, ln = tid & 63;
-    const int wm = wv & 1, wn = wv >> 1;
-    const int lm = ln & 15, lq = ln >> 4;
-    const int sr = tid >> 2, sq = tid & 3;
-
-    const _Float16* asrc = A + (size_t)(m0 + sr) * K + sq * 8;
-    const _Float16* bsrc = (n0 + sr < N) ? (Bt + (size_t)(n0 + sr) * K + sq * 8) : zbuf;
-
-    f32x4 acc[2][2];
-#pragma unroll
-    for (int i = 0; i < 2; ++i)
-#pragma unroll
-        for (int j = 0; j < 2; ++j) acc[i][j] = (f32x4){0.f, 0.f, 0.f, 0.f};
-
-    const int NT = K >> 5;
-    GEMM_STAGE(0, 0);
-#pragma unroll 1
-    for (int it = 0; it < NT; ++it) {
-        const int bi = it & 1;
-        if (it + 1 < NT) {
-            GEMM_STAGE((it + 1) * 32, bi ^ 1);
-            asm volatile("s_waitcnt vmcnt(2)" ::: "memory");
-        } else {
-            asm volatile("s_waitcnt vmcnt(0)" ::: "memory");
-        }
-        __builtin_amdgcn_s_barrier();
-        f16x8 af[2], bf[2];
-#pragma unroll
-        for (int mt = 0; mt < 2; ++mt) af[mt] = *(const f16x8*)&aS[bi][(wm * 32 + mt * 16 + lm) * 32 + lq * 8];
-#pragma unroll
-        for (int nt = 0; nt < 2; ++nt) bf[nt] = *(const f16x8*)&bS[bi][(wn * 32 + nt * 16 + lm) * 32 + lq * 8];
-#pragma unroll
-        for (int mt = 0; mt < 2; ++mt)
-#pragma unroll
-            for (int nt = 0; nt < 2; ++nt)
-                acc[mt][nt] = __builtin_amdgcn_mfma_f32_16x16x32_f16(af[mt], bf[nt], acc[mt][nt], 0, 0, 0);
-        __builtin_amdgcn_sched_barrier(0);
-        __builtin_amdgcn_s_barrier();
-    }
-
-#pragma unroll
-    for (int mt = 0; mt < 2; ++mt) {
-#pragma unroll
-        for (int nt = 0; nt < 2; ++nt) {
-            int col = n0 + wn * 32 + nt * 16 + lm;
-            if (col >= N) continue;
-#pragma unroll
-            for (int r = 0; r < 4; ++r) {
-                int row = m0 + wm * 32 + mt * 16 + lq * 4 + r;
-                C[(size_t)row * ldC + col] = acc[mt][nt][r];
-            }
-        }
-    }
+    const float* __restrict__ boxes, const float* __restrict__ scales,
+    const float* __restrict__ pdls, const float* __restrict__ pdts,
+    const u32* __restrict__ meta, u32* __restrict__ gpartC)
+{
+    __shared__ __attribute__((aligned(16))) char smem[16384];
+    const int bid = blockIdx.x;
+    if (bid >= 512) {
+        histC_256(boxes, scales, pdls, pdts, meta, gpartC, bid - 512, smem);
+        return;
+    }
+    const int z = bid >> 8, rem = bid & 255;
+    const int n0 = (rem & 7) * 64, m0 = (rem >> 3) * 64;
+    gemm_body<0, float>(fusion, z ? WgcT : WgrT, zbuf, nullptr, z ? C1 : C0,
+                        512, 768, 512, n0, m0,
+                        (_Float16*)smem, (_Float16*)(smem + 8192));
 }
 
 __global__ __launch_bounds__(256) void gemm16h_kernel(
@@ -431,74 +544,14 @@
     float* __restrict__ C0, float* __restrict__ C1,
     int M, int N0, int N1, int K)
 {
+    __shared__ __attribute__((aligned(16))) char smem[16384];
     const int z = blockIdx.z;
-    const _Float16* __restrict__ A  = z ? A1 : A0;
-    const _Float16* __restrict__ Bt = z ? Bt1 : Bt0;
-    const float* __restrict__ bias  = z ? bias1 : bias0;
-    float* __restrict__ C           = z ? C1 : C0;
     const int N = z ? N1 : N0;
-    const int ldC = N;
     const int n0 = blockIdx.x * 64, m0 = blockIdx.y * 64;
     if (n0 >= N) return;
-    __shared__ _Float16 aS[2][256 * 8];
-    __shared__ _Float16 bS[2][256 * 8];
-    const int tid = threadIdx.x;
-    const int wv = tid >> 6, ln = tid & 63;
-    const int wm = wv & 1, wn = wv >> 1;
-    const int lm = ln & 15, lq = ln >> 4;
-    const int sr = tid >> 2, sq = tid & 3;
-
-    const _Float16* asrc = A + (size_t)(m0 + sr) * K + sq * 8;
-    const _Float16* bsrc = (n0 + sr < N) ? (Bt + (size_t)(n0 + sr) * K + sq * 8) : zbuf;
-
-    f32x4 acc[2][2];
-#pragma unroll
-    for (int i = 0; i < 2; ++i)
-#pragma unroll
-        for (int j = 0; j < 2; ++j) acc[i][j] = (f32x4){0.f, 0.f, 0.f, 0.f};
-
-    const int NT = K >> 5;
-    GEMM_STAGE(0, 0);
-#pragma unroll 1
-    for (int it = 0; it < NT; ++it) {
-        const int bi = it & 1;
-        if (it + 1 < NT) {
-            GEMM_STAGE((it + 1) * 32, bi ^ 1);
-            asm volatile("s_waitcnt vmcnt(2)" ::: "memory");
-        } else {
-            asm volatile("s_waitcnt vmcnt(0)" ::: "memory");
-        }
-        __builtin_amdgcn_s_barrier();
-        f16x8 af[2], bf[2];
-#pragma unroll
-        for (int mt = 0; mt < 2; ++mt) af[mt] = *(const f16x8*)&aS[bi][(wm * 32 + mt * 16 + lm) * 32 + lq * 8];
-#pragma unroll
-        for (int nt = 0; nt < 2; ++nt) bf[nt] = *(const f16x8*)&bS[bi][(wn * 32 + nt * 16 + lm) * 32 + lq * 8];
-#pragma unroll
-        for (int mt = 0; mt < 2; ++mt)
-#pragma unroll
-            for (int nt = 0; nt < 2; ++nt)
-                acc[mt][nt] = __builtin_amdgcn_mfma_f32_16x16x32_f16(af[mt], bf[nt], acc[mt][nt], 0, 0, 0);
-        __builtin_amdgcn_sched_barrier(0);
-        __builtin_amdgcn_s_barrier();
-    }
-
-#pragma unroll
-    for (int mt = 0; mt < 2; ++mt) {
-#pragma unroll
-        for (int nt = 0; nt < 2; ++nt) {
-            int col = n0 + wn * 32 + nt * 16 + lm;
-            if (col >= N) continue;
-            float bs = bias[col];
-#pragma unroll
-            for (int r = 0; r < 4; ++r) {
-                int row = m0 + wm * 32 + mt * 16 + lq * 4 + r;
-                float v = acc[mt][nt][r] + bs;
-                v = (v >= 0.f) ? v : 0.01f * v;
-                C[(size_t)row * ldC + col] = v;
-            }
-        }
-    }
+    gemm_body<2, float>(z ? A1 : A0, z ? Bt1 : Bt0, zbuf, z ? bias1 : bias0,
+                        z ? C1 : C0, N, K, N, n0, m0,
+                        (_Float16*)smem, (_Float16*)(smem + 8192));
 }
 
 __device__ __forceinline__ float compute_sv_tb(
@@ -525,156 +578,6 @@
     float tbv = red[0];
     __syncthreads();
     return tbv;
-}
-
-#define QBITS(e, QB)                                                   \
-    {                                                                  \
-        int i_ = (e) / 511; int jj_ = (e) - i_ * 511;                  \
-        int j_ = jj_ + (jj_ >= i_ ? 1 : 0);                            \
-        float diff_ = sv[i_] - sv[j_];                                 \
-        float u_ = (diff_ * 5.0f) / tbv;                               \
-        float q_ = u_ * u_;                                            \
-        QB = __float_as_uint(q_);                                      \
-    }
-
-__global__ __launch_bounds__(1024) void histA_kernel(
-    const float* __restrict__ boxes, const float* __restrict__ scales,
-    const float* __restrict__ pdls, const float* __restrict__ pdts,
-    u32* __restrict__ gpart)
-{
-    __shared__ float sv[512]; __shared__ float red[512];
-    __shared__ u32 lh[4096];
-    const int sel = blockIdx.y, b = sel >> 1, t = sel & 1;
-    const int tid = threadIdx.x;
-    for (int i = tid; i < 4096; i += 1024) lh[i] = 0;
-    const float tbv = compute_sv_tb(boxes, scales, pdls, pdts, b, t, sv, red);
-    const int e1 = min((int)(blockIdx.x + 1) * ECHUNK, NE);
-    for (int e = blockIdx.x * ECHUNK + tid; e < e1; e += 1024) {
-        u32 qb; QBITS(e, qb);
-        atomicAdd(&lh[qb >> 20], 1u);
-    }
-    __syncthreads();
-    u32* G = gpart + ((size_t)sel * NCHUNK + blockIdx.x) * 4096;
-    for (int i = tid; i < 4096; i += 1024) G[i] = lh[i];
-}
-
-__global__ __launch_bounds__(1024) void scanA_kernel(
-    const u32* __restrict__ gpart, u32* __restrict__ meta)
-{
-    const int sel = blockIdx.x, tid = threadIdx.x;
-    __shared__ u32 bins[4096];
-    __shared__ u32 sc[2][1024];
-    for (int b = tid; b < 4096; b += 1024) {
-        u32 s = 0;
-        for (int c = 0; c < NCHUNK; ++c) s += gpart[((size_t)sel * NCHUNK + c) * 4096 + b];
-        bins[b] = s;
-    }
-    __syncthreads();
-    u32 part = 0;
-#pragma unroll
-    for (int j = 0; j < 4; ++j) part += bins[tid * 4 + j];
-    sc[0][tid] = part;
-    __syncthreads();
-    int src = 0;
-    for (int st = 1; st < 1024; st <<= 1) {
-        sc[1 - src][tid] = sc[src][tid] + (tid >= st ? sc[src][tid - st] : 0);
-        __syncthreads(); src = 1 - src;
-    }
-    u32 inc = sc[src][tid], exc = inc - part;
-    if (exc < (u32)KEDGE && (u32)KEDGE <= inc) {
-        u32 cum = exc;
-        for (int j = 0; j < 4; ++j) {
-            u32 c = bins[tid * 4 + j];
-            if (cum + c >= (u32)KEDGE) {
-                meta[sel * MS + 0] = (u32)(tid * 4 + j);
-                meta[sel * MS + 1] = (u32)KEDGE - cum;
-                break;
-            }
-            cum += c;
-        }
-    }
-}
-
-__global__ __launch_bounds__(1024) void histB_kernel(
-    const float* __restrict__ boxes, const float* __restrict__ scales,
-    const float* __restrict__ pdls, const float* __restrict__ pdts,
-    const u32* __restrict__ meta, u32* __restrict__ gpart)
-{
-    __shared__ float sv[512]; __shared__ float red[512];
-    __shared__ u32 lh[4096];
-    const int sel = blockIdx.y, b = sel >> 1, t = sel & 1;
-    const int tid = threadIdx.x;
-    for (int i = tid; i < 4096; i += 1024) lh[i] = 0;
-    const float tbv = compute_sv_tb(boxes, scales, pdls, pdts, b, t, sv, red);
-    const u32 p12 = meta[sel * MS + 0];
-    const int e1 = min((int)(blockIdx.x + 1) * ECHUNK, NE);
-    for (int e = blockIdx.x * ECHUNK + tid; e < e1; e += 1024) {
-        u32 qb; QBITS(e, qb);
-        if ((qb >> 20) == p12) atomicAdd(&lh[(qb >> 8) & 0xFFF], 1u);
-    }
-    __syncthreads();
-    u32* G = gpart + ((size_t)sel * NCHUNK + blockIdx.x) * 4096;
-    for (int i = tid; i < 4096; i += 1024) G[i] = lh[i];
-}
-
-__global__ __launch_bounds__(1024) void scanB_kernel(
-    const u32* __restrict__ gpart, u32* __restrict__ meta)
-{
-    const int sel = blockIdx.x, tid = threadIdx.x;
-    const u32 TH = meta[sel * MS + 1];
-    __shared__ u32 bins[4096];
-    __shared__ u32 sc[2][1024];
-    for (int b = tid; b < 4096; b += 1024) {
-        u32 s = 0;
-        for (int c = 0; c < NCHUNK; ++c) s += gpart[((size_t)sel * NCHUNK + c) * 4096 + b];
-        bins[b] = s;
-    }
-    __syncthreads();
-    u32 part = 0;
-#pragma unroll
-    for (int j = 0; j < 4; ++j) part += bins[tid * 4 + j];
-    sc[0][tid] = part;
-    __syncthreads();
-    int src = 0;
-    for (int st = 1; st < 1024; st <<= 1) {
-        sc[1 - src][tid] = sc[src][tid] + (tid >= st ? sc[src][tid - st] : 0);
-        __syncthreads(); src = 1 - src;
-    }
-    u32 inc = sc[src][tid], exc = inc - part;
-    if (exc < TH && TH <= inc) {
-        u32 cum = exc;
-        for (int j = 0; j < 4; ++j) {
-            u32 c = bins[tid * 4 + j];
-            if (cum + c >= TH) {
-                meta[sel * MS + 6] = (meta[sel * MS + 0] << 12) | (u32)(tid * 4 + j);
-                meta[sel * MS + 7] = TH - cum;
-                break;
-            }
-            cum += c;
-        }
-    }
-}
-
-__global__ __launch_bounds__(1024) void histC_kernel(
-    const float* __restrict__ boxes, const float* __restrict__ scales,
-    const float* __restrict__ pdls, const float* __restrict__ pdts,
-    const u32* __restrict__ meta, u32* __restrict__ gpart)
-{
-    __shared__ float sv[512]; __shared__ float red[512];
-    __shared__ u32 lh[256];
-    const int sel = blockIdx.y, b = sel >> 1, t = sel & 1;
-    const int tid = threadIdx.x;
-    if (tid < 256) lh[tid] = 0;
-    const float tbv = compute_sv_tb(boxes, scales, pdls, pdts, b, t, sv, red);
-    const u32 p24 = meta[sel * MS + 6];
-    const int e1 = min((int)(blockIdx.x + 1) * ECHUNK, NE);
-    for (int e = blockIdx.x * ECHUNK + tid; e < e1; e += 1024) {
-        u32 qb; QBITS(e, qb);
-        if ((qb >> 8) == p24) atomicAdd(&lh[qb & 0xFF], 1u);
-    }
-    __syncthreads();
-    u32* G = gpart + ((size_t)sel * NCHUNK + blockIdx.x) * 256;
-    if (tid < 256) G[tid] = lh[tid];
 }
 
 __global__ __launch_bounds__(256) void scanC_kernel(
@@ -931,22 +834,21 @@
     prep_kernel<<<4800, 256, 0, stream>>>(x, xf16, W_dec, wf16,
                                           W_cnn, WcT, W_grow, WgrT, W_gcol, WgcT,
                                           W_rcls, WrT, W_ccls, WccT);
-    conv_part_kernel<<<dim3(768), 256, 0, stream>>>(xf16, wf16, zbuf, pbuf);
-    conv_sum_kernel<<<2304, 256, 0, stream>>>(pbuf, b_dec, dec);
-    roi_box_kernel<<<2048, 256, 0, stream>>>(dec, boxes, W_box, b_box, cnn, fusion);
-    gemm16_kernel<1, _Float16><<<dim3(8, 32), 256, 0, stream>>>(cnn, WcT, zbuf, b_cnn, fusion + 256, 2048, 512, 1024, 768);
-    histA_kernel<<<dim3(NCHUNK, 8), 1024, 0, stream>>>(boxes, scales, pdls, pdts, gpartA);
-    scanA_kernel<<<8, 1024, 0, stream>>>(gpartA, meta);
-    histB_kernel<<<dim3(NCHUNK, 8), 1024, 0, stream>>>(boxes, scales, pdls, pdts, meta, gpartB);
-    scanB_kernel<<<8, 1024, 0, stream>>>(gpartB, meta);
-    histC_kernel<<<dim3(NCHUNK, 8), 1024, 0, stream>>>(boxes, scales, pdls, pdts, meta, gpartC);
+    conv_histA_kernel<<<1024, 256, 0, stream>>>(xf16, wf16, zbuf, pbuf,
+                                                boxes, scales, pdls, pdts, gpartA);
+    sum_scanA_kernel<<<2312, 256, 0, stream>>>(pbuf, b_dec, dec, gpartA, meta);
+    roi_histB_kernel<<<2304, 256, 0, stream>>>(dec, boxes, W_box, b_box, cnn, fusion,
+                                               scales, pdls, pdts, meta, gpartB);
+    gemmcnn_scanB_kernel<<<264, 256, 0, stream>>>(cnn, WcT, zbuf, b_cnn, fusion + 256,
+                                                  gpartB, meta);
+    gemmz_histC_kernel<<<768, 256, 0, stream>>>(fusion, WgrT, WgcT, zbuf,
+                                                xw, xw + 1048576,
+                                                boxes, scales, pdls, pdts, meta, gpartC);
     scanC_kernel<<<8, 256, 0, stream>>>(gpartC, meta);
     emit_kernel<<<dim3(NCHUNK, 8), 1024, 0, stream>>>(boxes, scales, pdls, pdts, meta,
                                                       tiebuf, tiecnt, es, ed, ewt, indeg, degw);
     tie_scan_fill_kernel<<<2, 1024, 0, stream>>>(meta, tiebuf, tiecnt, es, ed, ewt,
                                                  indeg, degw, offsA, dis, csr);
-    gemm16z_kernel<<<dim3(8, 32, 2), 256, 0, stream>>>(fusion, WgrT, WgcT, zbuf, xw, xw + 1048576,
-                                                       2048, 512, 768, 512);
     gcn_agg_kernel<<<dim3(2048, 2), 256, 0, stream>>>(xw, xw + 1048576, b_grow, b_gcol,
                                                       es, ewt, csr, offsA, indeg, dis,
                                                       feats, feats + (size_t)2048 * 512);
```
